# Optimization experiments

Hardware: AMD Instinct MI355X
Metric: run time of the kernel (lower is better)

Reference implementation:

```python
import jax, jax.numpy as jnp
import numpy as np
import math

C = 128
A_SCALES = [2.0, 4.0, 8.0]
A_RATIOS = [0.5, 1.0, 2.0]
STRIDES = [4, 8, 16, 32, 64]
NA = len(A_SCALES) * len(A_RATIOS)
IMG = 1024
N = 2
NMS_THRESH = 0.7
NUM_PRE = 6000
NUM_POST = 300
SCALE_CLIP = math.log(1000.0 / 16.0)


def base_anchors(stride):
    c = stride / 2.0
    a = []
    for s in A_SCALES:
        for r in A_RATIOS:
            h = stride * s * math.sqrt(r)
            w = stride * s * math.sqrt(1.0 / r)
            a.append((c - h / 2.0, c - w / 2.0, c + h / 2.0, c + w / 2.0))
    return np.array(a, dtype=np.float32)  # [NA,4] yxyx


def shifted_anchors(stride, H, W):
    base = jnp.asarray(base_anchors(stride))
    gy = jnp.arange(H, dtype=jnp.float32) * stride
    gx = jnp.arange(W, dtype=jnp.float32) * stride
    grid = jnp.stack(jnp.meshgrid(gy, gx, indexing='ij'), axis=-1)  # [H,W,2]
    shift = jnp.concatenate([grid, grid], axis=-1)  # [H,W,4]
    return (base[None, None] + shift[:, :, None]).reshape(-1, 4)  # [H*W*NA,4]


def conv(x, w, b, pad):
    y = jax.lax.conv_general_dilated(x, w, (1, 1), pad, dimension_numbers=('NCHW', 'OIHW', 'NCHW'))
    return y + b[None, :, None, None]


def head(x, w1, b1, wobj, bobj, wbbx, bbbx):
    h = jax.nn.relu(conv(x, w1, b1, 'SAME'))
    obj = conv(h, wobj, bobj, 'VALID')  # [N,NA,H,W]
    bbx = conv(h, wbbx, bbbx, 'VALID')  # [N,4*NA,H,W]
    n = x.shape[0]
    obj = obj.transpose(0, 2, 3, 1).reshape(n, -1)       # (h,w,anchor) order
    bbx = bbx.transpose(0, 2, 3, 1).reshape(n, -1, 4)
    return obj, bbx


def shift_boxes(anchors, deltas):
    yx = (anchors[..., :2] + anchors[..., 2:]) * 0.5
    hw = anchors[..., 2:] - anchors[..., :2]
    yx_o = yx + deltas[..., :2] * hw
    hw_o = hw * jnp.exp(jnp.minimum(deltas[..., 2:], SCALE_CLIP))
    return jnp.concatenate([yx_o - 0.5 * hw_o, yx_o + 0.5 * hw_o], axis=-1)


def nms_single(boxes, scores):
    # greedy hard NMS; boxes [P,4] yxyx, scores [P]; fixed NUM_POST outputs
    areas = (boxes[:, 2] - boxes[:, 0]) * (boxes[:, 3] - boxes[:, 1])

    def step(active, _):
        masked = jnp.where(active, scores, -jnp.inf)
        i = jnp.argmax(masked)
        ok = active[i]
        tl = jnp.maximum(boxes[i, :2], boxes[:, :2])
        br = jnp.minimum(boxes[i, 2:], boxes[:, 2:])
        inter = jnp.clip(br[:, 0] - tl[:, 0], 0.0) * jnp.clip(br[:, 1] - tl[:, 1], 0.0)
        iou = inter / (areas[i] + areas - inter + 1e-9)
        active = active & (iou <= NMS_THRESH)
        return active, (jnp.where(ok, i, 0), ok)

    _, (idx, valid) = jax.lax.scan(step, jnp.ones(boxes.shape[0], bool), None, length=NUM_POST)
    return idx, valid


def forward(x0, x1, x2, x3, x4, w1, b1, wobj, bobj, wbbx, bbbx, valid_size):
    feats = [x0, x1, x2, x3, x4]
    objs, bbxs, ancs = [], [], []
    for f, s in zip(feats, STRIDES):
        o, b = head(f, w1, b1, wobj, bobj, wbbx, bbbx)
        objs.append(o)
        bbxs.append(b)
        ancs.append(shifted_anchors(s, f.shape[2], f.shape[3]))
    obj = jnp.concatenate(objs, axis=1)        # [N,M]
    bbx = jnp.concatenate(bbxs, axis=1)        # [N,M,4]
    anchors = jnp.concatenate(ancs, axis=0)    # [M,4]
    boxes = shift_boxes(anchors[None], bbx)    # [N,M,4]
    h = valid_size[:, 0].astype(boxes.dtype)[:, None]
    w = valid_size[:, 1].astype(boxes.dtype)[:, None]
    boxes = jnp.stack([jnp.clip(boxes[..., 0], 0.0, h),
                       jnp.clip(boxes[..., 1], 0.0, w),
                       jnp.clip(boxes[..., 2], 0.0, h),
                       jnp.clip(boxes[..., 3], 0.0, w)], axis=-1)
    k = min(boxes.shape[1], NUM_PRE)
    top_scores, top_idx = jax.lax.top_k(obj, k)                     # per-image topk
    top_boxes = jnp.take_along_axis(boxes, top_idx[..., None], axis=1)
    idx, valid = jax.vmap(nms_single)(jax.lax.stop_gradient(top_boxes),
                                      jax.lax.stop_gradient(top_scores))
    props = jnp.take_along_axis(top_boxes, idx[..., None], axis=1)  # [N,NUM_POST,4]
    props = props * valid[..., None].astype(props.dtype)            # zero-pad invalid
    return props, valid


def setup_inputs() -> dict:
    key = jax.random.key(0)
    ks = jax.random.split(key, 8)
    sizes = [IMG // s for s in STRIDES]
    inp = {}
    for i, hw in enumerate(sizes):
        inp['x%d' % i] = jax.random.normal(ks[i], (N, C, hw, hw), jnp.float32)
    inp['w1'] = jax.random.normal(ks[5], (C, C, 3, 3), jnp.float32) * 0.05
    inp['b1'] = jnp.zeros((C,), jnp.float32)
    inp['wobj'] = jax.random.normal(ks[6], (NA, C, 1, 1), jnp.float32) * 0.05
    inp['bobj'] = jnp.zeros((NA,), jnp.float32)
    inp['wbbx'] = jax.random.normal(ks[7], (4 * NA, C, 1, 1), jnp.float32) * 0.05
    inp['bbbx'] = jnp.zeros((4 * NA,), jnp.float32)
    inp['valid_size'] = jnp.array([[IMG, IMG]] * N, jnp.int32)
    return inp


def reference(x0, x1, x2, x3, x4, w1, b1, wobj, bobj, wbbx, bbbx, valid_size):
    return forward(x0, x1, x2, x3, x4, w1, b1, wobj, bobj, wbbx, bbbx, valid_size)
```

## Files before the change

### kernel.cpp

```cpp
#include <hip/hip_runtime.h>
#include <stdint.h>
#include <math.h>

#define M_TOT 785664
#define NPRE  6000
#define NPOST 300
#define CAP   8192
#define NWORDS 94
#define ROWW   96
#define NPAD   6016

__device__ __forceinline__ uint32_t okey(float f) {
    uint32_t u = __float_as_uint(f);
    return (u & 0x80000000u) ? ~u : (u | 0x80000000u);
}

__global__ void k_init(const float* __restrict__ w1, float* __restrict__ wt,
                       uint32_t* __restrict__ p, int zn) {
    int i = blockIdx.x * 256 + threadIdx.x;
    if (i < zn) p[i] = 0u;
    if (i < 128 * 128 * 9) {
        int co = i / 1152; int r = i % 1152; int ci = r / 9; int tap = r % 9;
        wt[ci * 1152 + tap * 128 + co] = w1[i];
    }
}

__global__ __launch_bounds__(512) void k_conv(
    const float* __restrict__ x0, const float* __restrict__ x1,
    const float* __restrict__ x2, const float* __restrict__ x3,
    const float* __restrict__ x4,
    const float* __restrict__ wt, const float* __restrict__ b1,
    const float* __restrict__ wobj, const float* __restrict__ bobj,
    const float* __restrict__ wbbx, const float* __restrict__ bbbx,
    float* __restrict__ sc, float* __restrict__ dl)
{
    __shared__ __attribute__((aligned(16))) float sx[8][18][20];
    __shared__ __attribute__((aligned(16))) float sw[8 * 9 * 128];

    int b = blockIdx.x, L = 0;
    if (b >= 512) { b -= 512; L = 1;
        if (b >= 128) { b -= 128; L = 2;
            if (b >= 32) { b -= 32; L = 3;
                if (b >= 8) { b -= 8; L = 4; } } } }
    const float* xs = (L == 0) ? x0 : (L == 1) ? x1 : (L == 2) ? x2 : (L == 3) ? x3 : x4;
    const int scoff_[5] = {0, 589824, 737280, 774144, 783360};
    int Wl = 256 >> L; int Hl = Wl; int HW = Wl * Wl;
    int tpiSh = 8 - 2 * L;
    int n  = b >> tpiSh;
    int r  = b & ((1 << tpiSh) - 1);
    int txSh = 4 - L;
    int ty0 = r >> txSh, tx0 = r & ((1 << txSh) - 1);
    int y0 = ty0 << 4, x0c = tx0 << 4;
    const float* xin = xs + (size_t)n * 128 * HW;

    int t = threadIdx.x;
    int tx = t & 15;
    int ty = t >> 4;
    int py = ty >> 1, px = (ty & 1) << 3;

    float acc0[4][8], acc1[4][8];
#pragma unroll
    for (int c = 0; c < 4; ++c)
#pragma unroll
        for (int e = 0; e < 8; ++e) { acc0[c][e] = 0.f; acc1[c][e] = 0.f; }

    for (int cc0 = 0; cc0 < 128; cc0 += 8) {
        __syncthreads();
        for (int i = t; i < 2880; i += 512) {
            int ci = i / 360; int rm = i % 360; int rr = rm / 20; int cc = rm % 20;
            float v = 0.f;
            int gy = y0 - 1 + rr, gx = x0c - 1 + cc;
            if (cc < 18 && gy >= 0 && gy < Hl && gx >= 0 && gx < Wl)
                v = xin[(size_t)(cc0 + ci) * HW + (size_t)gy * Wl + gx];
            sx[ci][rr][cc] = v;
        }
        {
            const float4* wsrc = (const float4*)(wt + (size_t)cc0 * 1152);
            float4* wdst = (float4*)sw;
            for (int i = t; i < 2304; i += 512) wdst[i] = wsrc[i];
        }
        __syncthreads();

#pragma unroll 1
        for (int ci = 0; ci < 8; ++ci) {
#pragma unroll
            for (int dy = 0; dy < 3; ++dy) {
                const float* xr = &sx[ci][py + dy][px];
                float4 xa = *(const float4*)(xr);
                float4 xb = *(const float4*)(xr + 4);
                float4 xc = *(const float4*)(xr + 8);
                float win[12] = {xa.x, xa.y, xa.z, xa.w, xb.x, xb.y, xb.z, xb.w,
                                 xc.x, xc.y, xc.z, xc.w};
#pragma unroll
                for (int dx = 0; dx < 3; ++dx) {
                    const float* wr = &sw[(ci * 9 + dy * 3 + dx) * 128 + tx * 4];
                    float4 wa = *(const float4*)(wr);
                    float4 wb = *(const float4*)(wr + 64);
                    float wva[4] = {wa.x, wa.y, wa.z, wa.w};
                    float wvb[4] = {wb.x, wb.y, wb.z, wb.w};
#pragma unroll
                    for (int e = 0; e < 8; ++e) {
                        float xv = win[e + dx];
#pragma unroll
                        for (int c = 0; c < 4; ++c) {
                            acc0[c][e] = fmaf(wva[c], xv, acc0[c][e]);
                            acc1[c][e] = fmaf(wvb[c], xv, acc1[c][e]);
                        }
                    }
                }
            }
        }
    }

#pragma unroll
    for (int c = 0; c < 4; ++c) {
        float ba = b1[tx * 4 + c];
        float bb = b1[64 + tx * 4 + c];
#pragma unroll
        for (int e = 0; e < 8; ++e) {
            float v0 = acc0[c][e] + ba;
            float v1 = acc1[c][e] + bb;
            acc0[c][e] = v0 > 0.f ? v0 : 0.f;
            acc1[c][e] = v1 > 0.f ? v1 : 0.f;
        }
    }

    int gy = y0 + py;
    size_t ppos = (size_t)gy * Wl + x0c + px;
    size_t scbase = (size_t)n * M_TOT + scoff_[L];
    size_t dlbase = (size_t)n * 4 * (size_t)M_TOT + 4 * (size_t)scoff_[L];
    for (int a = 0; a < 45; ++a) {
        const float* wp = (a < 9) ? (wobj + (size_t)a * 128) : (wbbx + (size_t)(a - 9) * 128);
        float4 wa = *(const float4*)(wp + tx * 4);
        float4 wb = *(const float4*)(wp + 64 + tx * 4);
        float wva[4] = {wa.x, wa.y, wa.z, wa.w};
        float wvb[4] = {wb.x, wb.y, wb.z, wb.w};
        float p[8];
#pragma unroll
        for (int e = 0; e < 8; ++e) p[e] = 0.f;
#pragma unroll
        for (int c = 0; c < 4; ++c)
#pragma unroll
            for (int e = 0; e < 8; ++e) {
                p[e] = fmaf(wva[c], acc0[c][e], p[e]);
                p[e] = fmaf(wvb[c], acc1[c][e], p[e]);
            }
#pragma unroll
        for (int mm = 1; mm < 16; mm <<= 1)
#pragma unroll
            for (int e = 0; e < 8; ++e)
                p[e] += __shfl_xor(p[e], mm, 64);
        if (tx == 0) {
            float bias = (a < 9) ? bobj[a] : bbbx[a - 9];
            float4 o0 = make_float4(p[0] + bias, p[1] + bias, p[2] + bias, p[3] + bias);
            float4 o1 = make_float4(p[4] + bias, p[5] + bias, p[6] + bias, p[7] + bias);
            float* dst = (a < 9) ? (sc + scbase + (size_t)a * HW + ppos)
                                 : (dl + dlbase + (size_t)(a - 9) * HW + ppos);
            *(float4*)dst = o0;
            *(float4*)(dst + 4) = o1;
        }
    }
}

__global__ __launch_bounds__(256) void k_hist(const float* __restrict__ sc,
                                              uint32_t* __restrict__ hist) {
    __shared__ uint32_t lh[8192];
    int n = blockIdx.y;
    for (int i = threadIdx.x; i < 8192; i += 256) lh[i] = 0u;
    __syncthreads();
    const float* s = sc + (size_t)n * M_TOT;
    int stride = gridDim.x * 256;
    for (int i = blockIdx.x * 256 + threadIdx.x; i < M_TOT; i += stride)
        atomicAdd(&lh[okey(s[i]) >> 19], 1u);
    __syncthreads();
    for (int i = threadIdx.x; i < 8192; i += 256) {
        uint32_t v = lh[i];
        if (v) atomicAdd(&hist[n * 8192 + i], v);
    }
}

__global__ void k_subhist(const float* __restrict__ sc, const uint32_t* __restrict__ ctrl,
                          uint32_t* __restrict__ subh) {
    int i = blockIdx.x * blockDim.x + threadIdx.x;
    int stride = gridDim.x * blockDim.x;
    for (; i < 2 * M_TOT; i += stride) {
        int n = i >= M_TOT;
        uint32_t k = okey(sc[i]);
        if ((k >> 19) == ctrl[n * 8 + 0])
            atomicAdd(&subh[n * 8192 + ((k >> 6) & 0x1FFFu)], 1u);
    }
}

__global__ void k_scan(const uint32_t* __restrict__ hist, uint32_t* __restrict__ ctrl, int phase) {
    int n = blockIdx.x;
    const uint32_t* h = hist + n * 8192;
    uint32_t* c = ctrl + n * 8;
    __shared__ uint32_t tp[256];
    int t = threadIdx.x;
    uint32_t s = 0;
    for (int r = 0; r < 32; ++r) s += h[8191 - (t * 32 + r)];
    tp[t] = s;
    __syncthreads();
    if (t == 0) {
        uint32_t run = (phase == 0) ? 0u : c[1];
        for (int i = 0; i < 256; ++i) { uint32_t v = tp[i]; tp[i] = run; run += v; }
    }
    __syncthreads();
    uint32_t cum = tp[t];
    for (int r = 0; r < 32; ++r) {
        int j = 8191 - (t * 32 + r);
        uint32_t cc = h[j];
        if (cum < 6000u && cum + cc >= 6000u) {
            if (phase == 0) { c[0] = (uint32_t)j; c[1] = cum; }
            else            { c[2] = (c[0] << 19) | ((uint32_t)j << 6); }
        }
        cum += cc;
    }
}

__global__ void k_compact(const float* __restrict__ sc, uint32_t* __restrict__ ctrl,
                          uint64_t* __restrict__ cand) {
    int i = blockIdx.x * blockDim.x + threadIdx.x;
    int stride = gridDim.x * blockDim.x;
    const int scoff_[5] = {0, 589824, 737280, 774144, 783360};
    int lane = threadIdx.x & 63;
    for (; i < 2 * M_TOT; i += stride) {
        int n = i >= M_TOT;
        int q = n ? (i - M_TOT) : i;
        uint32_t k = okey(sc[i]);
        bool hit = (k >= ctrl[n * 8 + 2]);
        unsigned long long m = __ballot(hit);
        if (m) {
            int leader = __builtin_ctzll(m);
            uint32_t base = 0;
            if (lane == leader) base = atomicAdd(&ctrl[n * 8 + 3], (uint32_t)__popcll(m));
            base = (uint32_t)__shfl((int)base, leader, 64);
            if (hit) {
                uint32_t slot = base + (uint32_t)__popcll(m & ((1ull << lane) - 1ull));
                if (slot < CAP) {
                    int Lq = (q < 589824) ? 0 : (q < 737280) ? 1 : (q < 774144) ? 2
                            : (q < 783360) ? 3 : 4;
                    int r = q - scoff_[Lq];
                    int sh = 16 - 2 * Lq;
                    int a = r >> sh;
                    int pos = r & ((1 << sh) - 1);
                    uint32_t mm = (uint32_t)(scoff_[Lq] + pos * 9 + a);
                    cand[(size_t)n * CAP + slot] = ((uint64_t)k << 32) | (uint32_t)(~mm);
                }
            }
        }
    }
}

__global__ __launch_bounds__(256) void k_rank(const uint64_t* __restrict__ cand,
                                              const uint32_t* __restrict__ ctrl,
                                              uint64_t* __restrict__ sorted) {
    __shared__ uint64_t chunk[2048];
    int n = blockIdx.y;
    uint32_t cnt = ctrl[n * 8 + 3];
    if (cnt > CAP) cnt = CAP;
    const uint64_t* cb = cand + (size_t)n * CAP;
    uint64_t* sb = sorted + (size_t)n * CAP;
    int i = blockIdx.x * 256 + threadIdx.x;
    uint64_t key = (i < (int)cnt) ? cb[i] : 0ull;
    uint32_t rank = 0;
    for (uint32_t base = 0; base < cnt; base += 2048) {
        __syncthreads();
        for (int j = threadIdx.x; j < 2048; j += 256) {
            uint32_t idx = base + (uint32_t)j;
            chunk[j] = (idx < cnt) ? cb[idx] : 0ull;
        }
        __syncthreads();
        uint32_t lim = cnt - base; if (lim > 2048u) lim = 2048u;
        for (uint32_t j = 0; j < lim; ++j) rank += (chunk[j] > key) ? 1u : 0u;
    }
    if (i < (int)cnt && rank < CAP) sb[rank] = key;
}

__global__ void k_decode(const uint64_t* __restrict__ cand, const float* __restrict__ dl,
                         const int* __restrict__ vsz, float* __restrict__ boxes,
                         unsigned long long* __restrict__ degm) {
    int i = blockIdx.x * 256 + threadIdx.x;
    if (i >= 2 * NPRE) return;
    int n = i / NPRE, rk = i % NPRE;
    const int scoff_[5] = {0, 589824, 737280, 774144, 783360};
    uint64_t pk = cand[(size_t)n * CAP + rk];
    uint32_t m = ~(uint32_t)(pk & 0xFFFFFFFFull);
    int Lq = (m < 589824u) ? 0 : (m < 737280u) ? 1 : (m < 774144u) ? 2 : (m < 783360u) ? 3 : 4;
    int r = (int)m - scoff_[Lq];
    int pos = r / 9;
    int a = r - pos * 9;
    int Wl = 256 >> Lq;
    int y = pos >> (8 - Lq);
    int xx = pos & (Wl - 1);
    float stridef = (float)(4 << Lq);
    double sD = (double)(2 << (a / 3));
    double rD = ((a % 3) == 0) ? 0.5 : ((a % 3) == 1) ? 1.0 : 2.0;
    double hD = ((double)stridef * sD) * sqrt(rD);
    double wD = ((double)stridef * sD) * sqrt(1.0 / rD);
    double cD = (double)stridef / 2.0;
    float y1b = (float)(cD - hD / 2.0);
    float x1b = (float)(cD - wD / 2.0);
    float y2b = (float)(cD + hD / 2.0);
    float x2b = (float)(cD + wD / 2.0);
    float gy = (float)y * stridef;
    float gx = (float)xx * stridef;
    float ay1 = __fadd_rn(y1b, gy), ax1 = __fadd_rn(x1b, gx);
    float ay2 = __fadd_rn(y2b, gy), ax2 = __fadd_rn(x2b, gx);
    float cy = __fmul_rn(__fadd_rn(ay1, ay2), 0.5f);
    float cx = __fmul_rn(__fadd_rn(ax1, ax2), 0.5f);
    float ah = __fsub_rn(ay2, ay1);
    float aw = __fsub_rn(ax2, ax1);
    size_t HWl = (size_t)Wl * Wl;
    size_t db = (size_t)n * 4 * M_TOT + 4 * (size_t)scoff_[Lq] + (size_t)pos;
    float dy_ = dl[db + (size_t)(a * 4 + 0) * HWl];
    float dx_ = dl[db + (size_t)(a * 4 + 1) * HWl];
    float dh_ = dl[db + (size_t)(a * 4 + 2) * HWl];
    float dw_ = dl[db + (size_t)(a * 4 + 3) * HWl];
    float yo = __fadd_rn(cy, __fmul_rn(dy_, ah));
    float xo = __fadd_rn(cx, __fmul_rn(dx_, aw));
    const float SCLIPf = 4.135166556742356f;
    float ho = __fmul_rn(ah, (float)exp((double)fminf(dh_, SCLIPf)));
    float wo = __fmul_rn(aw, (float)exp((double)fminf(dw_, SCLIPf)));
    float hf = (float)vsz[n * 2 + 0], wf = (float)vsz[n * 2 + 1];
    float y1 = fminf(fmaxf(__fsub_rn(yo, __fmul_rn(0.5f, ho)), 0.f), hf);
    float x1 = fminf(fmaxf(__fsub_rn(xo, __fmul_rn(0.5f, wo)), 0.f), wf);
    float y2 = fminf(fmaxf(__fadd_rn(yo, __fmul_rn(0.5f, ho)), 0.f), hf);
    float x2 = fminf(fmaxf(__fadd_rn(xo, __fmul_rn(0.5f, wo)), 0.f), wf);
    *(float4*)(boxes + ((size_t)n * NPAD + rk) * 4) = make_float4(y1, x1, y2, x2);
    float area = __fmul_rn(__fsub_rn(y2, y1), __fsub_rn(x2, x1));
    float selfiou = __fdiv_rn(area, __fadd_rn(area, 1e-9f));
    if (!(selfiou > 0.7f))
        atomicOr(&degm[(size_t)n * ROWW + (rk >> 6)], 1ull << (rk & 63));
}

__global__ __launch_bounds__(256) void k_iou(const float* __restrict__ boxes,
                                             uint64_t* __restrict__ ioum) {
    int n = blockIdx.y;
    int i = blockIdx.x * 4 + (threadIdx.x >> 6);
    int lane = threadIdx.x & 63;
    const float* bsrc = boxes + (size_t)n * NPAD * 4;
    float4 bi = *(const float4*)(bsrc + (size_t)i * 4);
    float ai = __fmul_rn(__fsub_rn(bi.z, bi.x), __fsub_rn(bi.w, bi.y));
    uint64_t* row = ioum + ((size_t)n * NPAD + i) * ROWW;
    int w0 = i >> 6;
    for (int w = lane; w < w0; w += 64) row[w] = 0ull;
    for (int w = w0; w < NWORDS; ++w) {
        int j = (w << 6) | lane;
        bool pred = false;
        if (j > i && j < NPRE) {
            float4 bj = *(const float4*)(bsrc + (size_t)j * 4);
            float aj = __fmul_rn(__fsub_rn(bj.z, bj.x), __fsub_rn(bj.w, bj.y));
            float ty = fmaxf(bi.x, bj.x), tx2 = fmaxf(bi.y, bj.y);
            float by = fminf(bi.z, bj.z), bx2 = fminf(bi.w, bj.w);
            float ih = fmaxf(__fsub_rn(by, ty), 0.f), iw = fmaxf(__fsub_rn(bx2, tx2), 0.f);
            float inter = __fmul_rn(ih, iw);
            float den = __fadd_rn(__fsub_rn(__fadd_rn(ai, aj), inter), 1e-9f);
            float iou = __fdiv_rn(inter, den);
            pred = iou > 0.7f;
        }
        unsigned long long msk = __ballot(pred);
        if (lane == 0) row[w] = (uint64_t)msk;
    }
}

__global__ __launch_bounds__(64) void k_nms(const float* __restrict__ boxes,
                                            const uint64_t* __restrict__ ioum,
                                            const unsigned long long* __restrict__ degm,
                                            float* __restrict__ out) {
    int n = blockIdx.x;
    __shared__ uint64_t sup[NWORDS];
    __shared__ uint64_t deg[NWORDS];
    __shared__ int keepl[NPOST];
    int lane = threadIdx.x;
    for (int w = lane; w < NWORDS; w += 64) {
        sup[w] = 0ull;
        deg[w] = degm[(size_t)n * ROWW + w];
    }
    __syncthreads();
    int kept = 0;
    bool stop = false;
    for (int w = 0; w < NWORDS && kept < NPOST && !stop; ++w) {
        uint64_t vmask = (w == NWORDS - 1) ? ((1ull << 48) - 1ull) : ~0ull;
        uint64_t avail = (~sup[w]) & vmask;
        while (avail && kept < NPOST) {
            int bpos = __builtin_ctzll(avail);
            int i = (w << 6) | bpos;
            const uint64_t* row = ioum + ((size_t)n * NPAD + i) * ROWW;
            uint64_t r0 = row[lane];
            uint64_t r1 = (lane < NWORDS - 64) ? row[64 + lane] : 0ull;
            if (lane == 0) keepl[kept] = i;
            kept++;
            if ((deg[w] >> bpos) & 1ull) {
                if (lane == 0) { for (int k2 = kept; k2 < NPOST; ++k2) keepl[k2] = i; }
                kept = NPOST;
                stop = true;
                break;
            }
            sup[lane] |= r0;
            if (lane < NWORDS - 64) sup[64 + lane] |= r1;
            __syncthreads();
            avail = (~sup[w]) & vmask & ~((2ull << bpos) - 1ull);
        }
    }
    __syncthreads();
    for (int k = lane; k < NPOST; k += 64) {
        float4 bx = make_float4(0.f, 0.f, 0.f, 0.f);
        float vf = 0.f;
        if (k < kept) {
            int i = keepl[k];
            bx = *(const float4*)(boxes + ((size_t)n * NPAD + i) * 4);
            vf = 1.f;
        }
        *(float4*)(out + (size_t)n * 1200 + (size_t)k * 4) = bx;
        out[2400 + n * 300 + k] = vf;
    }
}

extern "C" void kernel_launch(void* const* d_in, const int* in_sizes, int n_in,
                              void* d_out, int out_size, void* d_ws, size_t ws_size,
                              hipStream_t stream) {
    (void)out_size; (void)ws_size;
    static const int want[12] = {16777216, 4194304, 1048576, 262144, 65536,
                                 147456, 128, 1152, 9, 4608, 36, 4};
    const void* p[12];
    for (int k = 0; k < 12; ++k) p[k] = d_in[k];
    bool pos_ok = (n_in >= 12);
    for (int k = 0; k < 12 && pos_ok; ++k) if (in_sizes[k] != want[k]) pos_ok = false;
    if (!pos_ok) {
        for (int k = 0; k < 12; ++k)
            for (int j = 0; j < n_in; ++j)
                if (in_sizes[j] == want[k]) { p[k] = d_in[j]; break; }
    }
    const float* x0   = (const float*)p[0];
    const float* x1   = (const float*)p[1];
    const float* x2   = (const float*)p[2];
    const float* x3   = (const float*)p[3];
    const float* x4   = (const float*)p[4];
    const float* w1   = (const float*)p[5];
    const float* b1   = (const float*)p[6];
    const float* wobj = (const float*)p[7];
    const float* bobj = (const float*)p[8];
    const float* wbbx = (const float*)p[9];
    const float* bbbx = (const float*)p[10];
    const int*   vsz  = (const int*)p[11];
    float* out = (float*)d_out;

    size_t off = 0;
    char* base = (char*)d_ws;
    auto carve = [&](size_t bytes) -> void* {
        void* q = base + off;
        off += (bytes + 255) & ~(size_t)255;
        return q;
    };
    float*    SC     = (float*)carve((size_t)2 * M_TOT * 4);
    float*    DL     = (float*)carve((size_t)2 * M_TOT * 16);
    float*    WT     = (float*)carve((size_t)147456 * 4);
    uint32_t* HIST   = (uint32_t*)carve((size_t)16384 * 4);
    uint32_t* SUBH   = (uint32_t*)carve((size_t)16384 * 4);
    uint32_t* CTRL   = (uint32_t*)carve((size_t)64 * 4);
    unsigned long long* DEGM = (unsigned long long*)carve((size_t)2 * ROWW * 8);
    uint64_t* CAND   = (uint64_t*)carve((size_t)2 * CAP * 8);
    uint64_t* SORTED = (uint64_t*)carve((size_t)2 * CAP * 8);
    float*    BOXES  = (float*)carve((size_t)2 * NPAD * 16);
    uint64_t* IOUM   = (uint64_t*)carve((size_t)2 * NPAD * ROWW * 8);

    int zn = (int)(((char*)CAND - (char*)HIST) / 4);
    int initN = (zn > 147456) ? zn : 147456;
    k_init<<<(initN + 255) / 256, 256, 0, stream>>>(w1, WT, HIST, zn);
    k_conv<<<682, 512, 0, stream>>>(x0, x1, x2, x3, x4, WT, b1,
                                    wobj, bobj, wbbx, bbbx, SC, DL);
    k_hist<<<dim3(256, 2), 256, 0, stream>>>(SC, HIST);
    k_scan<<<2, 256, 0, stream>>>(HIST, CTRL, 0);
    k_subhist<<<1024, 256, 0, stream>>>(SC, CTRL, SUBH);
    k_scan<<<2, 256, 0, stream>>>(SUBH, CTRL, 1);
    k_compact<<<1024, 256, 0, stream>>>(SC, CTRL, CAND);
    k_rank<<<dim3(CAP / 256, 2), 256, 0, stream>>>(CAND, CTRL, SORTED);
    k_decode<<<(2 * NPRE + 255) / 256, 256, 0, stream>>>(SORTED, DL, vsz, BOXES, DEGM);
    k_iou<<<dim3(NPRE / 4, 2), 256, 0, stream>>>(BOXES, IOUM);
    k_nms<<<2, 64, 0, stream>>>(BOXES, IOUM, DEGM, out);
}
```

Before: 1.049 ms.

## Precompute conv tile offsets, vectorize rank chunk loads, prefetch NMS IoU rows

Three independent changes. The conv input staging loop now computes its gather offsets once per block, replacing the integer div/mod work that ran every channel chunk. The rank kernel loads the candidate chunk with 128-bit loads and drops the bounds check, relying on the padded buffer beyond cnt being readable. The serial NMS loop predicts the next two surviving boxes and prefetches their IoU mask rows, so global load latency overlaps the current iteration. The prefetch adds extra loads that are wasted when a prediction misses.

```diff
diff --git a/kernel.cpp b/kernel.cpp
--- a/kernel.cpp
+++ b/kernel.cpp
@@ -58,6 +58,21 @@
     int ty = t >> 4;
     int py = ty >> 1, px = (ty & 1) << 3;
 
+    uint32_t soff[6];
+#pragma unroll
+    for (int k = 0; k < 6; ++k) {
+        int i = t + (k << 9);
+        uint32_t off = 0xFFFFFFFFu;
+        if (i < 2880) {
+            int ci = i / 360; int rm = i % 360; int rr = rm / 20; int cc = rm % 20;
+            int gy = y0 - 1 + rr, gx = x0c - 1 + cc;
+            if (cc < 18 && gy >= 0 && gy < Hl && gx >= 0 && gx < Wl)
+                off = (uint32_t)(ci * HW + gy * Wl + gx);
+        }
+        soff[k] = off;
+    }
+    float* sxf = (float*)sx;
+
     float acc0[4][8], acc1[4][8];
 #pragma unroll
     for (int c = 0; c < 4; ++c)
@@ -66,13 +81,11 @@
 
     for (int cc0 = 0; cc0 < 128; cc0 += 8) {
         __syncthreads();
-        for (int i = t; i < 2880; i += 512) {
-            int ci = i / 360; int rm = i % 360; int rr = rm / 20; int cc = rm % 20;
-            float v = 0.f;
-            int gy = y0 - 1 + rr, gx = x0c - 1 + cc;
-            if (cc < 18 && gy >= 0 && gy < Hl && gx >= 0 && gx < Wl)
-                v = xin[(size_t)(cc0 + ci) * HW + (size_t)gy * Wl + gx];
-            sx[ci][rr][cc] = v;
+#pragma unroll
+        for (int k = 0; k < 6; ++k) {
+            int i = t + (k << 9);
+            if (i < 2880)
+                sxf[i] = (soff[k] != 0xFFFFFFFFu) ? xin[(size_t)cc0 * HW + soff[k]] : 0.f;
         }
         {
             const float4* wsrc = (const float4*)(wt + (size_t)cc0 * 1152);
@@ -255,7 +268,7 @@
 __global__ __launch_bounds__(256) void k_rank(const uint64_t* __restrict__ cand,
                                               const uint32_t* __restrict__ ctrl,
                                               uint64_t* __restrict__ sorted) {
-    __shared__ uint64_t chunk[2048];
+    __shared__ __attribute__((aligned(16))) uint64_t chunk[2048];
     int n = blockIdx.y;
     uint32_t cnt = ctrl[n * 8 + 3];
     if (cnt > CAP) cnt = CAP;
@@ -264,12 +277,11 @@
     int i = blockIdx.x * 256 + threadIdx.x;
     uint64_t key = (i < (int)cnt) ? cb[i] : 0ull;
     uint32_t rank = 0;
+    const ulonglong2* cb2 = (const ulonglong2*)cb;
     for (uint32_t base = 0; base < cnt; base += 2048) {
         __syncthreads();
-        for (int j = threadIdx.x; j < 2048; j += 256) {
-            uint32_t idx = base + (uint32_t)j;
-            chunk[j] = (idx < cnt) ? cb[idx] : 0ull;
-        }
+        for (int j = threadIdx.x; j < 1024; j += 256)
+            ((ulonglong2*)chunk)[j] = cb2[(base >> 1) + j];
         __syncthreads();
         uint32_t lim = cnt - base; if (lim > 2048u) lim = 2048u;
         for (uint32_t j = 0; j < lim; ++j) rank += (chunk[j] > key) ? 1u : 0u;
@@ -380,15 +392,14 @@
     __syncthreads();
     int kept = 0;
     bool stop = false;
+    int pfi0 = -1, pfi1 = -1;
+    uint64_t pf00 = 0, pf01 = 0, pf10 = 0, pf11 = 0;
     for (int w = 0; w < NWORDS && kept < NPOST && !stop; ++w) {
         uint64_t vmask = (w == NWORDS - 1) ? ((1ull << 48) - 1ull) : ~0ull;
         uint64_t avail = (~sup[w]) & vmask;
         while (avail && kept < NPOST) {
             int bpos = __builtin_ctzll(avail);
             int i = (w << 6) | bpos;
-            const uint64_t* row = ioum + ((size_t)n * NPAD + i) * ROWW;
-            uint64_t r0 = row[lane];
-            uint64_t r1 = (lane < NWORDS - 64) ? row[64 + lane] : 0ull;
             if (lane == 0) keepl[kept] = i;
             kept++;
             if ((deg[w] >> bpos) & 1ull) {
@@ -396,6 +407,46 @@
                 kept = NPOST;
                 stop = true;
                 break;
+            }
+            uint64_t r0, r1;
+            if (i == pfi0)      { r0 = pf00; r1 = pf01; }
+            else if (i == pfi1) { r0 = pf10; r1 = pf11; }
+            else {
+                const uint64_t* row = ioum + ((size_t)n * NPAD + i) * ROWW;
+                r0 = row[lane];
+                r1 = (lane < NWORDS - 64) ? row[64 + lane] : 0ull;
+            }
+            int cand0 = -1, cand1 = -1;
+            if (w < 64) {
+                uint64_t candl = (~(sup[lane] | r0));
+                unsigned long long na = __shfl((unsigned long long)candl, w, 64);
+                na &= vmask & ~((2ull << bpos) - 1ull);
+                unsigned long long nb = 0;
+                if (w + 1 < 64) {
+                    uint64_t vm2 = (w + 1 == NWORDS - 1) ? ((1ull << 48) - 1ull) : ~0ull;
+                    nb = __shfl((unsigned long long)candl, w + 1, 64) & vm2;
+                }
+                if (na) {
+                    cand0 = (w << 6) | __builtin_ctzll(na);
+                    unsigned long long na2 = na & (na - 1);
+                    if (na2) cand1 = (w << 6) | __builtin_ctzll(na2);
+                    else if (nb) cand1 = ((w + 1) << 6) | __builtin_ctzll(nb);
+                } else if (nb) {
+                    cand0 = ((w + 1) << 6) | __builtin_ctzll(nb);
+                    unsigned long long nb2 = nb & (nb - 1);
+                    if (nb2) cand1 = ((w + 1) << 6) | __builtin_ctzll(nb2);
+                }
+            }
+            pfi0 = cand0; pfi1 = cand1;
+            if (pfi0 >= 0) {
+                const uint64_t* rw = ioum + ((size_t)n * NPAD + pfi0) * ROWW;
+                pf00 = rw[lane];
+                pf01 = (lane < NWORDS - 64) ? rw[64 + lane] : 0ull;
+            }
+            if (pfi1 >= 0) {
+                const uint64_t* rw = ioum + ((size_t)n * NPAD + pfi1) * ROWW;
+                pf10 = rw[lane];
+                pf11 = (lane < NWORDS - 64) ? rw[64 + lane] : 0ull;
             }
             sup[lane] |= r0;
             if (lane < NWORDS - 64) sup[64 + lane] |= r1;
```

New measurement: 1.161 ms. 1.11x slower.
